# Kernel tuning notes

Hardware: AMD Instinct MI355X
Metric: run time of the kernel (lower is better)

Reference implementation:

```python
import jax, jax.numpy as jnp
import numpy as np

N_NODES = 100000
NUM_FEAT = 64
NUM_CLASS = 40
N_EDGES = 1600000


def setup_inputs() -> dict:
    key = jax.random.key(0)
    k1, k2, k3, k4, k5 = jax.random.split(key, 5)
    x = jax.random.normal(k1, (N_NODES, NUM_FEAT), dtype=jnp.float32)
    index = jax.random.randint(k2, (2, N_EDGES), 0, N_NODES, dtype=jnp.int64)
    # SAGEConv params: lin_l applied to aggregated neighbors (has bias),
    # lin_r applied to root features (no bias) -- PyG convention.
    s = 1.0 / np.sqrt(NUM_FEAT)
    lin_l_w = jax.random.uniform(k3, (NUM_FEAT, NUM_CLASS), dtype=jnp.float32, minval=-s, maxval=s)
    lin_l_b = jnp.zeros((NUM_CLASS,), dtype=jnp.float32)
    lin_r_w = jax.random.uniform(k4, (NUM_FEAT, NUM_CLASS), dtype=jnp.float32, minval=-s, maxval=s)
    return {"x": x, "index": index, "lin_l_w": lin_l_w, "lin_l_b": lin_l_b, "lin_r_w": lin_r_w}


def reference(x, index, lin_l_w, lin_l_b, lin_r_w):
    src, dst = index[0], index[1]
    # Mean aggregation over incoming neighbors: messages flow src -> dst.
    msg = x[src]                                        # [E, F] gather
    agg_sum = jax.ops.segment_sum(msg, dst, num_segments=N_NODES)   # [N, F]
    deg = jax.ops.segment_sum(jnp.ones((index.shape[1],), dtype=x.dtype), dst,
                              num_segments=N_NODES)     # [N]
    agg = agg_sum / jnp.maximum(deg, 1.0)[:, None]      # mean, safe for isolated nodes
    out = agg @ lin_l_w + lin_l_b + x @ lin_r_w         # [N, C]
    return jax.nn.log_softmax(out, axis=1)
```

## Files before the change

### kernel.cpp

```cpp
#include <hip/hip_runtime.h>
#include <hip/hip_fp8.h>
#include <math.h>

constexpr int NODES = 100000;
constexpr int F = 64;
constexpr int C = 40;
constexpr int YPITCH = 64;
constexpr int NPB   = 64;
constexpr int NB    = (NODES + NPB - 1) / NPB;
constexpr int NBPAD = 2048;
constexpr int BCAP  = 1408;
constexpr int TILE  = 4096;
constexpr int NTILES = NODES / 16;
constexpr int MBLK  = (NTILES + 3) / 4;

typedef __attribute__((ext_vector_type(8))) short short8;
typedef __attribute__((ext_vector_type(4))) float floatx4;
typedef __attribute__((ext_vector_type(2))) float floatx2;
typedef __attribute__((ext_vector_type(4))) unsigned uintx4;
typedef __attribute__((ext_vector_type(4))) float fx4;

__device__ inline unsigned bf16pack2(float a, float b) {
    unsigned ua = __builtin_bit_cast(unsigned, a);
    unsigned ub = __builtin_bit_cast(unsigned, b);
    ua += 0x7FFFu + ((ua >> 16) & 1u);
    ub += 0x7FFFu + ((ub >> 16) & 1u);
    return (ua >> 16) | (ub & 0xFFFF0000u);
}
__device__ inline unsigned short bf16of(float a) {
    unsigned ua = __builtin_bit_cast(unsigned, a);
    ua += 0x7FFFu + ((ua >> 16) & 1u);
    return (unsigned short)(ua >> 16);
}
__device__ inline float bf16tof(unsigned short u) {
    return __builtin_bit_cast(float, (unsigned)u << 16);
}
__device__ inline unsigned char fp8of(float f) {
    __hip_fp8_e4m3 q(f);
    return (unsigned char)q.__x;
}
template <int K>
__device__ inline float fp8byte(unsigned d) {
    __hip_fp8_e4m3 v;
    v.__x = (__hip_fp8_storage_t)((d >> (8 * K)) & 0xFFu);
    return (float)v;
}
template <int HI>
__device__ inline floatx2 fp8pk(unsigned d) {
#if __has_builtin(__builtin_amdgcn_cvt_pk_f32_fp8)
    return __builtin_amdgcn_cvt_pk_f32_fp8((int)d, HI != 0);
#else
    floatx2 r;
    r[0] = fp8byte<HI ? 2 : 0>(d);
    r[1] = fp8byte<HI ? 3 : 1>(d);
    return r;
#endif
}

__global__ __launch_bounds__(256)
void fused_A(const float* __restrict__ x,
             const float* __restrict__ wl,
             const float* __restrict__ bl,
             const float* __restrict__ wr,
             const int* __restrict__ src, const int* __restrict__ dst,
             int* __restrict__ gcursor, int* __restrict__ bbuf, int nedges,
             unsigned char* __restrict__ y8f, unsigned short* __restrict__ z8) {
    __shared__ union {
        struct { int lhist[NB]; int lcur[NB]; } bz;
        struct { unsigned sB[10 * 64 * 4]; float sbl[40]; } mf;
    } sh;

    int t = threadIdx.x;

    if (blockIdx.x < MBLK) {
        if (t < 40) sh.mf.sbl[t] = bl[t];
        for (int s = t; s < 640; s += 256) {
            int region = s >> 6;
            int l      = s & 63;
            int ct = region >> 1, ks = region & 1;
            int col = ct * 16 + (l & 15);
            int fb  = ks * 32 + ((l >> 4) << 3);
            const float* wsrc = (col < 40) ? (wl + col) : (wr + (col - 40));
            unsigned* dstp = &sh.mf.sB[s * 4];
#pragma unroll
            for (int p = 0; p < 4; ++p) {
                float a = wsrc[(fb + 2 * p) * 40];
                float b = wsrc[(fb + 2 * p + 1) * 40];
                dstp[p] = bf16pack2(a, b);
            }
        }
        __syncthreads();

        int lane = t & 63;
        int nt = blockIdx.x * 4 + (t >> 6);
        if (nt >= NTILES) return;

        union U { unsigned u[4]; short8 v; };
        short8 bf[5][2];
#pragma unroll
        for (int ct = 0; ct < 5; ++ct)
#pragma unroll
            for (int ks = 0; ks < 2; ++ks) {
                U tmp;
                const uint4* p =
                    (const uint4*)&sh.mf.sB[((ct * 2 + ks) * 64 + lane) * 4];
                uint4 q = *p;
                tmp.u[0] = q.x; tmp.u[1] = q.y; tmp.u[2] = q.z; tmp.u[3] = q.w;
                bf[ct][ks] = tmp.v;
            }

        floatx4 acc[5];
#pragma unroll
        for (int ct = 0; ct < 5; ++ct) {
            int col = ct * 16 + (lane & 15);
            float bias = (col >= 40) ? sh.mf.sbl[col - 40] : 0.0f;
            acc[ct] = (floatx4){bias, bias, bias, bias};
        }

        int row = nt * 16 + (lane & 15);
        const fx4* xp = (const fx4*)(x + (size_t)row * F);
        short8 af[2];
#pragma unroll
        for (int ks = 0; ks < 2; ++ks) {
            int kb = ks * 8 + ((lane >> 4) << 1);
            fx4 va = __builtin_nontemporal_load(xp + kb);
            fx4 vb = __builtin_nontemporal_load(xp + kb + 1);
            U a;
            a.u[0] = bf16pack2(va[0], va[1]);
            a.u[1] = bf16pack2(va[2], va[3]);
            a.u[2] = bf16pack2(vb[0], vb[1]);
            a.u[3] = bf16pack2(vb[2], vb[3]);
            af[ks] = a.v;
        }

#pragma unroll
        for (int ks = 0; ks < 2; ++ks)
#pragma unroll
            for (int ct = 0; ct < 5; ++ct)
                acc[ct] = __builtin_amdgcn_mfma_f32_16x16x32_bf16(
                    af[ks], bf[ct][ks], acc[ct], 0, 0, 0);

#pragma unroll
        for (int ct = 0; ct < 5; ++ct) {
            int col = ct * 16 + (lane & 15);
#pragma unroll
            for (int r = 0; r < 4; ++r) {
                int grow = nt * 16 + ((lane >> 4) << 2) + r;
                if (col < 40) y8f[(size_t)grow * YPITCH + col] = fp8of(acc[ct][r]);
                else          z8[(size_t)grow * C + (col - 40)] = bf16of(acc[ct][r]);
            }
        }
    } else {
        for (int i = t; i < NB; i += 256) sh.bz.lhist[i] = 0;
        __syncthreads();

        int bb = blockIdx.x - MBLK;
        int base = bb * TILE;
        int pk[16], bk[16];
#pragma unroll
        for (int u = 0; u < 16; ++u) {
            int e = base + u * 256 + t;
            bk[u] = -1;
            if (e < nedges) {
                int s = __builtin_nontemporal_load(src + e);
                int d = __builtin_nontemporal_load(dst + e);
                if ((unsigned)s < (unsigned)NODES && (unsigned)d < (unsigned)NODES) {
                    bk[u] = d >> 6;
                    pk[u] = s | ((d & 63) << 17);
                    atomicAdd(&sh.bz.lhist[bk[u]], 1);
                }
            }
        }
        __syncthreads();
        for (int i = t; i < NB; i += 256) {
            int c = sh.bz.lhist[i];
            sh.bz.lcur[i] = c ? atomicAdd(&gcursor[i], c) : 0;
        }
        __syncthreads();
#pragma unroll
        for (int u = 0; u < 16; ++u) {
            if (bk[u] >= 0) {
                int p = atomicAdd(&sh.bz.lcur[bk[u]], 1);
                if (p < BCAP) bbuf[(size_t)bk[u] * BCAP + p] = pk[u];
            }
        }
    }
}

__device__ inline void acc8(float (&acc)[8], uint2 q) {
    floatx2 v;
    v = fp8pk<0>(q.x); acc[0] += v[0]; acc[1] += v[1];
    v = fp8pk<1>(q.x); acc[2] += v[0]; acc[3] += v[1];
    v = fp8pk<0>(q.y); acc[4] += v[0]; acc[5] += v[1];
    v = fp8pk<1>(q.y); acc[6] += v[0]; acc[7] += v[1];
}

__global__ __launch_bounds__(256)
void sort_aggregate(const unsigned char* __restrict__ y8f,
                    const unsigned short* __restrict__ z8,
                    const int* __restrict__ bbuf,
                    const int* __restrict__ gcount,
                    float* __restrict__ out) {
    __shared__ int lhist[NPB];
    __shared__ int lcur[NPB];
    __shared__ int slds[BCAP];

    int b = blockIdx.x;
    int t = threadIdx.x;

    if (t < NPB) lhist[t] = 0;
    __syncthreads();

    int cnt = gcount[b];
    if (cnt > BCAP) cnt = BCAP;
    const int* myb = bbuf + (size_t)b * BCAP;

    int ek[(BCAP + 255) / 256];
    int nh = 0;
    for (int i = t; i < cnt; i += 256) ek[nh++] = __builtin_nontemporal_load(myb + i);
#pragma unroll
    for (int u = 0; u < (BCAP + 255) / 256; ++u)
        if (u < nh) atomicAdd(&lhist[ek[u] >> 17], 1);
    __syncthreads();

    if (t < NPB) {
        int c = lhist[t];
        int sc = c;
#pragma unroll
        for (int d = 1; d < 64; d <<= 1) {
            int o = __shfl_up(sc, d);
            if (t >= d) sc += o;
        }
        lcur[t] = sc - c;
    }
    __syncthreads();

#pragma unroll
    for (int u = 0; u < (BCAP + 255) / 256; ++u)
        if (u < nh) {
            int pk = ek[u];
            int p = atomicAdd(&lcur[pk >> 17], 1);
            slds[p] = pk & 0x1FFFF;
        }
    __syncthreads();

    int gid = t >> 3;
    int i = t & 7;
    bool valid = (i < 5);
    int byteoff = (valid ? i : 4) * 8;

    for (int j = 0; j < 2; ++j) {
        int nd = gid * 2 + j;
        int n = b * NPB + nd;
        if (n >= NODES) break;

        int dg = lhist[nd];
        const int* sp = slds + (lcur[nd] - dg);

        uintx4 zv = {0u, 0u, 0u, 0u};
        if (valid) zv = __builtin_nontemporal_load(
                            (const uintx4*)(z8 + (size_t)n * C + i * 8));

        float acc[8] = {0.f, 0.f, 0.f, 0.f, 0.f, 0.f, 0.f, 0.f};

        int npair = dg >> 1;
        if (npair > 0) {
            int s0 = sp[0];
            int s1 = sp[1];
            for (int p = 0; p < npair; ++p) {
                int c0 = s0, c1 = s1;
                int nx = 2 * p + 2;
                int pi = (nx + 1 < dg) ? nx : dg - 2;
                s0 = sp[pi];
                s1 = sp[pi + 1];
                uint2 q0 = *(const uint2*)(y8f + (size_t)c0 * YPITCH + byteoff);
                uint2 q1 = *(const uint2*)(y8f + (size_t)c1 * YPITCH + byteoff);
                acc8(acc, q0);
                acc8(acc, q1);
            }
        }
        if (dg & 1) {
            int cl = sp[dg - 1];
            uint2 q = *(const uint2*)(y8f + (size_t)cl * YPITCH + byteoff);
            acc8(acc, q);
        }

        float inv = 1.0f / (float)(dg > 0 ? dg : 1);

        float o[8];
        if (valid) {
            unsigned zu[4] = {zv[0], zv[1], zv[2], zv[3]};
#pragma unroll
            for (int k = 0; k < 4; ++k) {
                o[2 * k]     = bf16tof((unsigned short)(zu[k] & 0xFFFFu))
                             + acc[2 * k] * inv;
                o[2 * k + 1] = bf16tof((unsigned short)(zu[k] >> 16))
                             + acc[2 * k + 1] * inv;
            }
        } else {
#pragma unroll
            for (int k = 0; k < 8; ++k) o[k] = -1e30f;
        }

        float mv = -1e30f;
        if (valid)
#pragma unroll
            for (int k = 0; k < 8; ++k) mv = fmaxf(mv, o[k]);
#pragma unroll
        for (int m = 1; m <= 4; m <<= 1) mv = fmaxf(mv, __shfl_xor(mv, m));

        float ev = 0.0f;
        if (valid)
#pragma unroll
            for (int k = 0; k < 8; ++k) ev += __expf(o[k] - mv);
#pragma unroll
        for (int m = 1; m <= 4; m <<= 1) ev += __shfl_xor(ev, m);
        float lse = mv + __logf(ev);

        if (valid) {
            fx4 o0 = {o[0] - lse, o[1] - lse, o[2] - lse, o[3] - lse};
            fx4 o1 = {o[4] - lse, o[5] - lse, o[6] - lse, o[7] - lse};
            fx4* op = (fx4*)(out + (size_t)n * C + i * 8);
            __builtin_nontemporal_store(o0, op);
            __builtin_nontemporal_store(o1, op + 1);
        }
    }
}

__global__ __launch_bounds__(256)
void scatter_kernel(const float* __restrict__ x, const int* __restrict__ src,
                    const int* __restrict__ dst, float* __restrict__ aggsum,
                    float* __restrict__ deg, int nedges) {
    int lane = threadIdx.x & 63;
    int e = blockIdx.x * 4 + (threadIdx.x >> 6);
    if (e >= nedges) return;
    int s = src[e], d = dst[e];
    if ((unsigned)s >= (unsigned)NODES || (unsigned)d >= (unsigned)NODES) return;
    atomicAdd(&aggsum[(size_t)d * F + lane], x[(size_t)s * F + lane]);
    if (lane == 0) atomicAdd(&deg[d], 1.0f);
}

__global__ __launch_bounds__(256)
void meanify_kernel(float* __restrict__ aggsum, const float* __restrict__ deg) {
    int lane = threadIdx.x & 63;
    int n = blockIdx.x * 4 + (threadIdx.x >> 6);
    if (n >= NODES) return;
    aggsum[(size_t)n * F + lane] *= 1.0f / fmaxf(deg[n], 1.0f);
}

__global__ __launch_bounds__(256)
void node_kernel(const float* __restrict__ x, const float* __restrict__ aggmean,
                 const float* __restrict__ wl, const float* __restrict__ bl,
                 const float* __restrict__ wr, float* __restrict__ out) {
    __shared__ alignas(16) float sWl[F * C];
    __shared__ alignas(16) float sWr[F * C];
    __shared__ alignas(16) float sb[C];
    for (int i = threadIdx.x; i < F * C; i += 256) { sWl[i] = wl[i]; sWr[i] = wr[i]; }
    if (threadIdx.x < C) sb[threadIdx.x] = bl[threadIdx.x];
    __syncthreads();
    int n = blockIdx.x * 256 + threadIdx.x;
    if (n >= NODES) return;
    float4 acc[10];
    const float4* sb4 = (const float4*)sb;
#pragma unroll
    for (int q = 0; q < 10; ++q) acc[q] = sb4[q];
    const float4* xr  = (const float4*)(x       + (size_t)n * F);
    const float4* ar  = (const float4*)(aggmean + (size_t)n * F);
    const float4* wl4 = (const float4*)sWl;
    const float4* wr4 = (const float4*)sWr;
    for (int f4 = 0; f4 < F / 4; ++f4) {
        float4 xv = xr[f4], av = ar[f4];
        float xs[4]  = {xv.x, xv.y, xv.z, xv.w};
        float as_[4] = {av.x, av.y, av.z, av.w};
#pragma unroll
        for (int jj = 0; jj < 4; ++jj) {
            int f = f4 * 4 + jj;
#pragma unroll
            for (int q = 0; q < 10; ++q) {
                float4 wlv = wl4[f * 10 + q], wrv = wr4[f * 10 + q];
                acc[q].x = fmaf(as_[jj], wlv.x, fmaf(xs[jj], wrv.x, acc[q].x));
                acc[q].y = fmaf(as_[jj], wlv.y, fmaf(xs[jj], wrv.y, acc[q].y));
                acc[q].z = fmaf(as_[jj], wlv.z, fmaf(xs[jj], wrv.z, acc[q].z));
                acc[q].w = fmaf(as_[jj], wlv.w, fmaf(xs[jj], wrv.w, acc[q].w));
            }
        }
    }
    float m = -1e30f;
#pragma unroll
    for (int q = 0; q < 10; ++q)
        m = fmaxf(m, fmaxf(fmaxf(acc[q].x, acc[q].y), fmaxf(acc[q].z, acc[q].w)));
    float ssum = 0.0f;
#pragma unroll
    for (int q = 0; q < 10; ++q)
        ssum += __expf(acc[q].x - m) + __expf(acc[q].y - m) +
                __expf(acc[q].z - m) + __expf(acc[q].w - m);
    float lse = m + __logf(ssum);
    float4* op = (float4*)(out + (size_t)n * C);
#pragma unroll
    for (int q = 0; q < 10; ++q) {
        float4 v;
        v.x = acc[q].x - lse; v.y = acc[q].y - lse;
        v.z = acc[q].z - lse; v.w = acc[q].w - lse;
        op[q] = v;
    }
}

extern "C" void kernel_launch(void* const* d_in, const int* in_sizes, int n_in,
                              void* d_out, int out_size, void* d_ws, size_t ws_size,
                              hipStream_t stream) {
    const float* x     = (const float*)d_in[0];
    const int*   index = (const int*)d_in[1];
    const float* wl    = (const float*)d_in[2];
    const float* bl    = (const float*)d_in[3];
    const float* wr    = (const float*)d_in[4];
    float* out = (float*)d_out;

    int nedges = in_sizes[1] / 2;
    const int* src = index;
    const int* dst = index + nedges;

    size_t need = (size_t)NODES * C * 2 + (size_t)NODES * YPITCH
                + ((size_t)NB * BCAP + NBPAD) * 4;

    if (ws_size >= need) {
        unsigned short* z8 = (unsigned short*)d_ws;
        unsigned char* y8f = (unsigned char*)(z8 + (size_t)NODES * C);
        int* bbuf       = (int*)(y8f + (size_t)NODES * YPITCH);
        int* gcursor    = bbuf + (size_t)NB * BCAP;

        hipMemsetAsync(gcursor, 0, NBPAD * sizeof(int), stream);

        int bblocks = (nedges + TILE - 1) / TILE;
        fused_A<<<MBLK + bblocks, 256, 0, stream>>>(
            x, wl, bl, wr, src, dst, gcursor, bbuf, nedges, y8f, z8);
        sort_aggregate<<<NB, 256, 0, stream>>>(
            y8f, z8, bbuf, gcursor, out);
    } else {
        float* aggsum = (float*)d_ws;
        float* deg    = aggsum + (size_t)NODES * F;
        hipMemsetAsync(d_ws, 0,
                       ((size_t)NODES * F + NODES) * sizeof(float), stream);
        scatter_kernel<<<(nedges + 3) / 4, 256, 0, stream>>>(
            x, src, dst, aggsum, deg, nedges);
        meanify_kernel<<<(NODES + 3) / 4, 256, 0, stream>>>(aggsum, deg);
        node_kernel<<<(NODES + 255) / 256, 256, 0, stream>>>(
            x, aggsum, wl, bl, wr, out);
    }
}
```

Measured before the change: 148.0 us.

## Bucket edges into 128-node buckets, each sorted and aggregated by two blocks

The bucketing stage now groups edges by destination into 128-node buckets instead of 64, halving the bucket count and the global cursor atomics. The aggregate kernel launches two blocks per bucket. Each block reads the whole bucket but keeps only edges for its 64-node half, then sorts and aggregates those locally. This cuts the per-bucket histogram/cursor contention in the scatter phase, at the cost of each bucket's edge list being read twice. The z8 load also changes from nontemporal to a normal load.

```diff
diff --git a/kernel.cpp b/kernel.cpp
--- a/kernel.cpp
+++ b/kernel.cpp
@@ -6,10 +6,12 @@
 constexpr int F = 64;
 constexpr int C = 40;
 constexpr int YPITCH = 64;
-constexpr int NPB   = 64;
+constexpr int NPB   = 128;
 constexpr int NB    = (NODES + NPB - 1) / NPB;
-constexpr int NBPAD = 2048;
-constexpr int BCAP  = 1408;
+constexpr int NBPAD = 1024;
+constexpr int BCAP  = 2816;
+constexpr int SCAP  = 1408;
+constexpr int EK    = (BCAP + 255) / 256;
 constexpr int TILE  = 4096;
 constexpr int NTILES = NODES / 16;
 constexpr int MBLK  = (NTILES + 3) / 4;
@@ -165,8 +167,8 @@
                 int s = __builtin_nontemporal_load(src + e);
                 int d = __builtin_nontemporal_load(dst + e);
                 if ((unsigned)s < (unsigned)NODES && (unsigned)d < (unsigned)NODES) {
-                    bk[u] = d >> 6;
-                    pk[u] = s | ((d & 63) << 17);
+                    bk[u] = d >> 7;
+                    pk[u] = s | ((d & 127) << 17);
                     atomicAdd(&sh.bz.lhist[bk[u]], 1);
                 }
             }
@@ -201,29 +203,36 @@
                     const int* __restrict__ bbuf,
                     const int* __restrict__ gcount,
                     float* __restrict__ out) {
-    __shared__ int lhist[NPB];
-    __shared__ int lcur[NPB];
-    __shared__ int slds[BCAP];
-
-    int b = blockIdx.x;
+    __shared__ int lhist[64];
+    __shared__ int lcur[64];
+    __shared__ int slds[SCAP];
+
+    int b    = blockIdx.x >> 1;
+    int half = blockIdx.x & 1;
     int t = threadIdx.x;
 
-    if (t < NPB) lhist[t] = 0;
+    if (t < 64) lhist[t] = 0;
     __syncthreads();
 
     int cnt = gcount[b];
     if (cnt > BCAP) cnt = BCAP;
     const int* myb = bbuf + (size_t)b * BCAP;
 
-    int ek[(BCAP + 255) / 256];
-    int nh = 0;
-    for (int i = t; i < cnt; i += 256) ek[nh++] = __builtin_nontemporal_load(myb + i);
-#pragma unroll
-    for (int u = 0; u < (BCAP + 255) / 256; ++u)
-        if (u < nh) atomicAdd(&lhist[ek[u] >> 17], 1);
+    int ek[EK];
+#pragma unroll
+    for (int u = 0; u < EK; ++u) {
+        int i = t + u * 256;
+        ek[u] = (i < cnt) ? myb[i] : -1;
+    }
+#pragma unroll
+    for (int u = 0; u < EK; ++u) {
+        int pk = ek[u];
+        if (pk >= 0 && ((pk >> 17) >> 6) == half)
+            atomicAdd(&lhist[(pk >> 17) & 63], 1);
+    }
     __syncthreads();
 
-    if (t < NPB) {
+    if (t < 64) {
         int c = lhist[t];
         int sc = c;
 #pragma unroll
@@ -236,12 +245,13 @@
     __syncthreads();
 
 #pragma unroll
-    for (int u = 0; u < (BCAP + 255) / 256; ++u)
-        if (u < nh) {
-            int pk = ek[u];
-            int p = atomicAdd(&lcur[pk >> 17], 1);
-            slds[p] = pk & 0x1FFFF;
-        }
+    for (int u = 0; u < EK; ++u) {
+        int pk = ek[u];
+        if (pk >= 0 && ((pk >> 17) >> 6) == half) {
+            int p = atomicAdd(&lcur[(pk >> 17) & 63], 1);
+            if (p < SCAP) slds[p] = pk & 0x1FFFF;
+        }
+    }
     __syncthreads();
 
     int gid = t >> 3;
@@ -251,15 +261,14 @@
 
     for (int j = 0; j < 2; ++j) {
         int nd = gid * 2 + j;
-        int n = b * NPB + nd;
+        int n = b * NPB + half * 64 + nd;
         if (n >= NODES) break;
 
         int dg = lhist[nd];
         const int* sp = slds + (lcur[nd] - dg);
 
         uintx4 zv = {0u, 0u, 0u, 0u};
-        if (valid) zv = __builtin_nontemporal_load(
-                            (const uintx4*)(z8 + (size_t)n * C + i * 8));
+        if (valid) zv = *(const uintx4*)(z8 + (size_t)n * C + i * 8);
 
         float acc[8] = {0.f, 0.f, 0.f, 0.f, 0.f, 0.f, 0.f, 0.f};
 
@@ -433,7 +442,7 @@
         int bblocks = (nedges + TILE - 1) / TILE;
         fused_A<<<MBLK + bblocks, 256, 0, stream>>>(
             x, wl, bl, wr, src, dst, gcursor, bbuf, nedges, y8f, z8);
-        sort_aggregate<<<NB, 256, 0, stream>>>(
+        sort_aggregate<<<NB * 2, 256, 0, stream>>>(
             y8f, z8, bbuf, gcursor, out);
     } else {
         float* aggsum = (float*)d_ws;
```

Result: faster. 144.2 us (-2.5%).
